# Optimization experiments

Measured on AMD Instinct MI355X. Metric: run time of the kernel, lower is better.

## Reference

```python
import jax, jax.numpy as jnp
import numpy as np

N = 50000      # nodes
E = 800000     # edges
IN = 128       # in_channels
H = 128        # hidden_channels
OUT = 40       # out_channels (classes)
EPS = 1e-5     # LayerNorm eps


def _glorot(key, fan_in, fan_out):
    lim = np.sqrt(6.0 / (fan_in + fan_out)).astype(np.float32)
    return jax.random.uniform(key, (fan_in, fan_out), jnp.float32, -lim, lim)


def setup_inputs() -> dict:
    key = jax.random.key(0)
    ks = jax.random.split(key, 8)
    x = jax.random.normal(ks[0], (N, IN), jnp.float32)
    edge_index = jax.random.randint(ks[1], (2, E), 0, N, jnp.int32)
    return {
        "x": x,
        "W0": _glorot(ks[2], IN, H), "b0": jnp.zeros((H,), jnp.float32),
        "W1": _glorot(ks[3], H, H),  "b1": jnp.zeros((H,), jnp.float32),
        "W2": _glorot(ks[4], H, OUT), "b2": jnp.zeros((OUT,), jnp.float32),
        "ln1_g": jnp.ones((H,), jnp.float32), "ln1_b": jnp.zeros((H,), jnp.float32),
        "ln2_g": jnp.ones((H,), jnp.float32), "ln2_b": jnp.zeros((H,), jnp.float32),
        "edge_index": edge_index,
    }


def reference(x, W0, b0, W1, b1, W2, b2, ln1_g, ln1_b, ln2_g, ln2_b, edge_index):
    # GCN normalization with self-loops: A_hat = D^-1/2 (A + I) D^-1/2
    self_idx = jnp.arange(N, dtype=edge_index.dtype)
    src = jnp.concatenate([edge_index[0], self_idx])  # [E+N]
    dst = jnp.concatenate([edge_index[1], self_idx])
    deg = jax.ops.segment_sum(jnp.ones_like(src, jnp.float32), dst, num_segments=N)
    dinv = jax.lax.rsqrt(deg)  # deg >= 1 thanks to self-loops
    norm = dinv[src] * dinv[dst]  # [E+N]

    def conv(h, W, b):
        h = h @ W                                  # [N, F] dense GEMM
        msg = h[src] * norm[:, None]               # gather + scale [E+N, F]
        return jax.ops.segment_sum(msg, dst, num_segments=N) + b

    def layernorm(h, g, b):
        mu = jnp.mean(h, axis=-1, keepdims=True)
        var = jnp.mean(jnp.square(h - mu), axis=-1, keepdims=True)
        return (h - mu) * jax.lax.rsqrt(var + EPS) * g + b

    # layer 0 (note: original uses lns[i+1], so lns[0] is never applied)
    h = jax.nn.relu(layernorm(conv(x, W0, b0), ln1_g, ln1_b))
    # dropout is identity in eval mode
    h = jax.nn.relu(layernorm(conv(h, W1, b1), ln2_g, ln2_b))
    h = conv(h, W2, b2)
    return jax.nn.log_softmax(h, axis=-1)
```

## Files before the change

### kernel.cpp

```cpp
#include <hip/hip_runtime.h>
#include <math.h>

typedef __attribute__((ext_vector_type(8))) short bf16x8;
typedef __attribute__((ext_vector_type(4))) float f32x4;
typedef unsigned short u16;
typedef unsigned int u32;

static __device__ __forceinline__ u16 f2bf(float f) {
    unsigned u = __float_as_uint(f);
    unsigned r = (u + 0x7fff + ((u >> 16) & 1)) >> 16;
    return (u16)r;
}
static __device__ __forceinline__ float bf2f(u16 h) {
    return __uint_as_float(((unsigned)h) << 16);
}
static __device__ __forceinline__ float pk_lo(u32 u) { return __uint_as_float(u << 16); }
static __device__ __forceinline__ float pk_hi(u32 u) { return __uint_as_float(u & 0xffff0000u); }

__global__ void init_k(int* __restrict__ counts, int n, int gN,
                       const float* __restrict__ W0, const float* __restrict__ W1,
                       const float* __restrict__ W2,
                       u16* __restrict__ w0hi, u16* __restrict__ w0lo,
                       u16* __restrict__ w1hi, u16* __restrict__ w1lo,
                       u16* __restrict__ w2hi, u16* __restrict__ w2lo) {
    int b = blockIdx.x;
    if (b < gN) {
        int i = b * 256 + threadIdx.x;
        if (i < n) counts[i] = 0;
        return;
    }
    int i = (b - gN) * 256 + threadIdx.x;
    const float* W; u16 *hi, *lo; int COLS, cin, idx;
    if (i < 16384)      { W = W0; hi = w0hi; lo = w0lo; COLS = 128; cin = 128; idx = i; }
    else if (i < 32768) { W = W1; hi = w1hi; lo = w1lo; COLS = 128; cin = 128; idx = i - 16384; }
    else if (i < 40960) { W = W2; hi = w2hi; lo = w2lo; COLS = 64;  cin = 40;  idx = i - 32768; }
    else return;
    int k = idx / COLS, col = idx % COLS;
    float v = (col < cin) ? W[k * cin + col] : 0.f;
    u16 h = f2bf(v);
    u16 l = f2bf(v - bf2f(h));
    int ct = col >> 4, ks = k >> 5, ln = (col & 15) + (((k >> 3) & 3) << 4), j = k & 7;
    int pos = (((ct * 4 + ks) * 64 + ln) << 3) + j;
    hi[pos] = h; lo[pos] = l;
}

__global__ void count_rank_k(const int* __restrict__ dst, int* __restrict__ counts,
                             u16* __restrict__ rank, int e) {
    int i = blockIdx.x * 256 + threadIdx.x;
    if (i < e) rank[i] = (u16)atomicAdd(&counts[dst[i]], 1);
}
__global__ __launch_bounds__(1024) void scan1_k(const int* __restrict__ counts,
                                                int* __restrict__ offs,
                                                int* __restrict__ bsum,
                                                float* __restrict__ dinv, int n) {
    __shared__ int ws[16];
    int tid = threadIdx.x;
    int i = blockIdx.x * 1024 + tid;
    int lane = tid & 63, w = tid >> 6;
    int c = (i < n) ? counts[i] : 0;
    if (i < n) dinv[i] = rsqrtf((float)c + 1.0f);
    int s = c;
#pragma unroll
    for (int o = 1; o < 64; o <<= 1) { int t = __shfl_up(s, o); if (lane >= o) s += t; }
    if (lane == 63) ws[w] = s;
    __syncthreads();
    if (w == 0) {
        int x = (lane < 16) ? ws[lane] : 0;
#pragma unroll
        for (int o = 1; o < 16; o <<= 1) { int t = __shfl_up(x, o); if (lane >= o) x += t; }
        if (lane < 16) ws[lane] = x;
    }
    __syncthreads();
    int base = (w > 0) ? ws[w - 1] : 0;
    int incl = base + s;
    if (i < n) offs[i + 1] = incl;
    if (tid == 1023) bsum[blockIdx.x] = incl;
}
__global__ void scan23_k(int* __restrict__ offs, const int* __restrict__ bsum,
                         int nb, int n) {
    __shared__ int pre[64];
    int tid = threadIdx.x;
    if (tid < 64) {
        int v = (tid < nb) ? bsum[tid] : 0;
#pragma unroll
        for (int o = 1; o < 64; o <<= 1) { int t = __shfl_up(v, o); if (tid >= o) v += t; }
        pre[tid] = v;
    }
    __syncthreads();
    int i = blockIdx.x * 256 + tid;
    if (i == 0) offs[0] = 0;
    if (i < n) {
        int b = i >> 10;
        offs[i + 1] += (b > 0) ? pre[b - 1] : 0;
    }
}

__global__ __launch_bounds__(256) void fill_gemm1_k(const int* __restrict__ src,
                                                    const int* __restrict__ dst,
                                                    const u16* __restrict__ rank,
                                                    const int* __restrict__ offs,
                                                    u16* __restrict__ csr, int e, int fillBlocks,
                                                    const float* __restrict__ A,
                                                    const u16* __restrict__ Whi,
                                                    const u16* __restrict__ Wlo,
                                                    const float* __restrict__ dinv,
                                                    u16* __restrict__ C, int nrows) {
    if ((int)blockIdx.x < fillBlocks) {
        int i = blockIdx.x * 256 + threadIdx.x;
        if (i < e) csr[offs[dst[i]] + (int)rank[i]] = (u16)src[i];
        return;
    }
    constexpr int COLS = 128;
    int bid = blockIdx.x - fillBlocks;
    int wave = threadIdx.x >> 6, lane = threadIdx.x & 63;
    int r0 = bid * 64 + wave * 16;
    int arow = min(r0 + (lane & 15), nrows - 1);
    int kbase = (lane >> 4) * 8;

    bf16x8 ahi[4], alo[4];
#pragma unroll
    for (int ks = 0; ks < 4; ++ks) {
        const float* ap = &A[(long)arow * 128 + ks * 32 + kbase];
        float4 f0 = *(const float4*)ap;
        float4 f1 = *(const float4*)(ap + 4);
        float fv[8] = {f0.x, f0.y, f0.z, f0.w, f1.x, f1.y, f1.z, f1.w};
#pragma unroll
        for (int j = 0; j < 8; ++j) {
            u16 h = f2bf(fv[j]);
            ahi[ks][j] = (short)h;
            alo[ks][j] = (short)f2bf(fv[j] - bf2f(h));
        }
    }
    float dscale[4];
#pragma unroll
    for (int r = 0; r < 4; ++r) {
        int orow = r0 + (lane >> 4) * 4 + r;
        dscale[r] = (orow < nrows) ? dinv[orow] : 0.f;
    }
#pragma unroll
    for (int ct = 0; ct < COLS / 16; ct += 2) {
        f32x4 acc0 = {0.f, 0.f, 0.f, 0.f}, acc1 = {0.f, 0.f, 0.f, 0.f};
#pragma unroll
        for (int ks = 0; ks < 4; ++ks) {
            int fo0 = ((ct * 4 + ks) * 64 + lane) * 8;
            int fo1 = (((ct + 1) * 4 + ks) * 64 + lane) * 8;
            bf16x8 bhi0 = *(const bf16x8*)&Whi[fo0];
            bf16x8 blo0 = *(const bf16x8*)&Wlo[fo0];
            bf16x8 bhi1 = *(const bf16x8*)&Whi[fo1];
            bf16x8 blo1 = *(const bf16x8*)&Wlo[fo1];
            acc0 = __builtin_amdgcn_mfma_f32_16x16x32_bf16(ahi[ks], bhi0, acc0, 0, 0, 0);
            acc1 = __builtin_amdgcn_mfma_f32_16x16x32_bf16(ahi[ks], bhi1, acc1, 0, 0, 0);
            acc0 = __builtin_amdgcn_mfma_f32_16x16x32_bf16(alo[ks], bhi0, acc0, 0, 0, 0);
            acc1 = __builtin_amdgcn_mfma_f32_16x16x32_bf16(alo[ks], bhi1, acc1, 0, 0, 0);
            acc0 = __builtin_amdgcn_mfma_f32_16x16x32_bf16(ahi[ks], blo0, acc0, 0, 0, 0);
            acc1 = __builtin_amdgcn_mfma_f32_16x16x32_bf16(ahi[ks], blo1, acc1, 0, 0, 0);
        }
#pragma unroll
        for (int r = 0; r < 4; ++r) {
            int orow = r0 + (lane >> 4) * 4 + r;
            if (orow < nrows) {
                C[(long)orow * COLS + ct * 16 + (lane & 15)] = f2bf(acc0[r] * dscale[r]);
                C[(long)orow * COLS + (ct + 1) * 16 + (lane & 15)] = f2bf(acc1[r] * dscale[r]);
            }
        }
    }
}

template<int COLS>
__global__ __launch_bounds__(256) void mfma_gemm_bf16a_k(const u16* __restrict__ A,
                                                         const u16* __restrict__ Whi,
                                                         const u16* __restrict__ Wlo,
                                                         const float* __restrict__ dinv,
                                                         u16* __restrict__ C, int nrows) {
    int wave = threadIdx.x >> 6, lane = threadIdx.x & 63;
    int r0 = blockIdx.x * 64 + wave * 16;
    int arow = min(r0 + (lane & 15), nrows - 1);
    int kbase = (lane >> 4) * 8;

    bf16x8 a[4];
#pragma unroll
    for (int ks = 0; ks < 4; ++ks)
        a[ks] = *(const bf16x8*)&A[(long)arow * 128 + ks * 32 + kbase];

    float dscale[4];
#pragma unroll
    for (int r = 0; r < 4; ++r) {
        int orow = r0 + (lane >> 4) * 4 + r;
        dscale[r] = (orow < nrows) ? dinv[orow] : 0.f;
    }
#pragma unroll
    for (int ct = 0; ct < COLS / 16; ct += 2) {
        f32x4 acc0 = {0.f, 0.f, 0.f, 0.f}, acc1 = {0.f, 0.f, 0.f, 0.f};
#pragma unroll
        for (int ks = 0; ks < 4; ++ks) {
            int fo0 = ((ct * 4 + ks) * 64 + lane) * 8;
            int fo1 = (((ct + 1) * 4 + ks) * 64 + lane) * 8;
            bf16x8 bhi0 = *(const bf16x8*)&Whi[fo0];
            bf16x8 blo0 = *(const bf16x8*)&Wlo[fo0];
            bf16x8 bhi1 = *(const bf16x8*)&Whi[fo1];
            bf16x8 blo1 = *(const bf16x8*)&Wlo[fo1];
            acc0 = __builtin_amdgcn_mfma_f32_16x16x32_bf16(a[ks], bhi0, acc0, 0, 0, 0);
            acc1 = __builtin_amdgcn_mfma_f32_16x16x32_bf16(a[ks], bhi1, acc1, 0, 0, 0);
            acc0 = __builtin_amdgcn_mfma_f32_16x16x32_bf16(a[ks], blo0, acc0, 0, 0, 0);
            acc1 = __builtin_amdgcn_mfma_f32_16x16x32_bf16(a[ks], blo1, acc1, 0, 0, 0);
        }
#pragma unroll
        for (int r = 0; r < 4; ++r) {
            int orow = r0 + (lane >> 4) * 4 + r;
            if (orow < nrows) {
                C[(long)orow * COLS + ct * 16 + (lane & 15)] = f2bf(acc0[r] * dscale[r]);
                C[(long)orow * COLS + (ct + 1) * 16 + (lane & 15)] = f2bf(acc1[r] * dscale[r]);
            }
        }
    }
}

__global__ __launch_bounds__(256) void agg_ln_relu_k(const u16* __restrict__ Cs,
                                                     const int* __restrict__ offs,
                                                     const u16* __restrict__ csr,
                                                     const float* __restrict__ dinv,
                                                     const float* __restrict__ bias,
                                                     const float* __restrict__ g,
                                                     const float* __restrict__ b,
                                                     u16* __restrict__ out, int n) {
    int wid = (blockIdx.x * 256 + threadIdx.x) >> 6;
    int lane = threadIdx.x & 63;
    if (wid >= n) return;
    const u32* C2 = (const u32*)Cs;
    u32 su = C2[(long)wid * 64 + lane];
    float axq[4], ayq[4];
    axq[0] = pk_lo(su); ayq[0] = pk_hi(su);
    axq[1] = axq[2] = axq[3] = 0.f;
    ayq[1] = ayq[2] = ayq[3] = 0.f;
    int beg = offs[wid], end = offs[wid + 1];
    int j = beg;
    while (j < end) {
        int take = min(64, end - j);
        int myidx = (lane < take) ? (int)csr[j + lane] : 0;
        int k = 0;
        for (; k + 16 <= take; k += 16) {
            int is[16];
#pragma unroll
            for (int q = 0; q < 16; ++q) is[q] = __shfl(myidx, k + q);
            u32 us[16];
#pragma unroll
            for (int q = 0; q < 16; ++q) us[q] = C2[(long)is[q] * 64 + lane];
#pragma unroll
            for (int q = 0; q < 16; ++q) {
                axq[q & 3] += pk_lo(us[q]);
                ayq[q & 3] += pk_hi(us[q]);
            }
        }
        for (; k + 8 <= take; k += 8) {
            int is[8];
#pragma unroll
            for (int q = 0; q < 8; ++q) is[q] = __shfl(myidx, k + q);
            u32 us[8];
#pragma unroll
            for (int q = 0; q < 8; ++q) us[q] = C2[(long)is[q] * 64 + lane];
#pragma unroll
            for (int q = 0; q < 8; ++q) {
                axq[q & 3] += pk_lo(us[q]);
                ayq[q & 3] += pk_hi(us[q]);
            }
        }
        for (; k < take; ++k) {
            int i0 = __shfl(myidx, k);
            u32 u0 = C2[(long)i0 * 64 + lane];
            axq[0] += pk_lo(u0); ayq[0] += pk_hi(u0);
        }
        j += take;
    }
    float ax = (axq[0] + axq[1]) + (axq[2] + axq[3]);
    float ay = (ayq[0] + ayq[1]) + (ayq[2] + ayq[3]);
    float w = dinv[wid];
    float2 bia = ((const float2*)bias)[lane];
    float t0 = ax * w + bia.x;
    float t1 = ay * w + bia.y;
    float s = t0 + t1;
#pragma unroll
    for (int off = 32; off; off >>= 1) s += __shfl_xor(s, off);
    float mu = s * (1.f / 128.f);
    float d0 = t0 - mu, d1 = t1 - mu;
    float v = d0 * d0 + d1 * d1;
#pragma unroll
    for (int off = 32; off; off >>= 1) v += __shfl_xor(v, off);
    float rstd = rsqrtf(v * (1.f / 128.f) + 1e-5f);
    float2 gv = ((const float2*)g)[lane];
    float2 bv = ((const float2*)b)[lane];
    float y0 = fmaxf(0.f, d0 * rstd * gv.x + bv.x);
    float y1 = fmaxf(0.f, d1 * rstd * gv.y + bv.y);
    ((u32*)out)[(long)wid * 64 + lane] = ((u32)f2bf(y1) << 16) | f2bf(y0);
}

__global__ __launch_bounds__(256) void agg_lsm_k(const u16* __restrict__ Cs,
                                                 const int* __restrict__ offs,
                                                 const u16* __restrict__ csr,
                                                 const float* __restrict__ dinv,
                                                 const float* __restrict__ b2,
                                                 float* __restrict__ out, int n) {
    int wid = (blockIdx.x * 256 + threadIdx.x) >> 6;
    int lane = threadIdx.x & 63;
    if (wid >= n) return;
    float aq[4];
    aq[0] = bf2f(Cs[(long)wid * 64 + lane]);
    aq[1] = aq[2] = aq[3] = 0.f;
    int beg = offs[wid], end = offs[wid + 1];
    int j = beg;
    while (j < end) {
        int take = min(64, end - j);
        int myidx = (lane < take) ? (int)csr[j + lane] : 0;
        int k = 0;
        for (; k + 16 <= take; k += 16) {
            int is[16];
#pragma unroll
            for (int q = 0; q < 16; ++q) is[q] = __shfl(myidx, k + q);
            u16 us[16];
#pragma unroll
            for (int q = 0; q < 16; ++q) us[q] = Cs[(long)is[q] * 64 + lane];
#pragma unroll
            for (int q = 0; q < 16; ++q) aq[q & 3] += bf2f(us[q]);
        }
        for (; k + 8 <= take; k += 8) {
            int is[8];
#pragma unroll
            for (int q = 0; q < 8; ++q) is[q] = __shfl(myidx, k + q);
            u16 us[8];
#pragma unroll
            for (int q = 0; q < 8; ++q) us[q] = Cs[(long)is[q] * 64 + lane];
#pragma unroll
            for (int q = 0; q < 8; ++q) aq[q & 3] += bf2f(us[q]);
        }
        for (; k < take; ++k) {
            int i0 = __shfl(myidx, k);
            aq[0] += bf2f(Cs[(long)i0 * 64 + lane]);
        }
        j += take;
    }
    float aa = (aq[0] + aq[1]) + (aq[2] + aq[3]);
    float v = (lane < 40) ? aa * dinv[wid] + b2[lane] : -INFINITY;
    float m = v;
#pragma unroll
    for (int off = 32; off; off >>= 1) m = fmaxf(m, __shfl_xor(m, off));
    float e = (lane < 40) ? expf(v - m) : 0.f;
    float s = e;
#pragma unroll
    for (int off = 32; off; off >>= 1) s += __shfl_xor(s, off);
    float r = v - m - logf(s);
    if (lane < 40) out[(long)wid * 40 + lane] = r;
}

extern "C" void kernel_launch(void* const* d_in, const int* in_sizes, int n_in,
                              void* d_out, int out_size, void* d_ws, size_t ws_size,
                              hipStream_t stream) {
    const float* x    = (const float*)d_in[0];
    const float* W0   = (const float*)d_in[1];
    const float* b0   = (const float*)d_in[2];
    const float* W1   = (const float*)d_in[3];
    const float* b1   = (const float*)d_in[4];
    const float* W2   = (const float*)d_in[5];
    const float* b2   = (const float*)d_in[6];
    const float* ln1g = (const float*)d_in[7];
    const float* ln1b = (const float*)d_in[8];
    const float* ln2g = (const float*)d_in[9];
    const float* ln2b = (const float*)d_in[10];
    const int*   ei   = (const int*)d_in[11];

    const int N = in_sizes[0] / 128;
    const int E = in_sizes[11] / 2;
    const int* esrc = ei;
    const int* edst = ei + E;
    float* out = (float*)d_out;

    const int Npad = ((N + 255) / 256) * 256;

    int* counts  = (int*)d_ws;
    int* offs    = counts + Npad;
    int* bsum    = offs + Npad;
    u16* rank16  = (u16*)(bsum + 64);
    u16* csr16   = rank16 + E;
    float* dinv  = (float*)(csr16 + E);
    u16* bufA    = (u16*)(dinv + Npad);
    u16* bufB    = bufA + (size_t)N * 128;
    u16* w0hi    = bufB + (size_t)N * 128;
    u16* w0lo    = w0hi + 16384;
    u16* w1hi    = w0lo + 16384;
    u16* w1lo    = w1hi + 16384;
    u16* w2hi    = w1lo + 16384;
    u16* w2lo    = w2hi + 8192;

    dim3 blk(256);
    int gN = (N + 255) / 256, gE = (E + 255) / 256;
    int nb1024 = (N + 1023) / 1024;
    int gG = (N + 63) / 64;
    int gW = (N + 3) / 4;

    init_k<<<gN + 160, blk, 0, stream>>>(counts, N, gN, W0, W1, W2,
                                         w0hi, w0lo, w1hi, w1lo, w2hi, w2lo);
    count_rank_k<<<gE, blk, 0, stream>>>(edst, counts, rank16, E);
    scan1_k<<<nb1024, 1024, 0, stream>>>(counts, offs, bsum, dinv, N);
    scan23_k<<<gN, blk, 0, stream>>>(offs, bsum, nb1024, N);
    fill_gemm1_k<<<gE + gG, blk, 0, stream>>>(esrc, edst, rank16, offs, csr16, E, gE,
                                              x, w0hi, w0lo, dinv, bufA, N);
    agg_ln_relu_k<<<gW, blk, 0, stream>>>(bufA, offs, csr16, dinv, b0, ln1g, ln1b, bufB, N);
    mfma_gemm_bf16a_k<128><<<gG, blk, 0, stream>>>(bufB, w1hi, w1lo, dinv, bufA, N);
    agg_ln_relu_k<<<gW, blk, 0, stream>>>(bufA, offs, csr16, dinv, b1, ln2g, ln2b, bufB, N);
    mfma_gemm_bf16a_k<64><<<gG, blk, 0, stream>>>(bufB, w2hi, w2lo, dinv, bufA, N);
    agg_lsm_k<<<gW, blk, 0, stream>>>(bufA, offs, csr16, dinv, b2, out, N);
}
```

Baseline: 211.4 us.

## Move first GEMM into count kernel and rescale with dinv in fill pass

The first-layer GEMM (x @ W0) now runs in the same launch as the edge-counting atomics, because it no longer needs dinv. It writes raw fp32 results to a scratch buffer. The CSR fill kernel then also applies the dinv row scaling and converts to bf16. This hides the GEMM behind the atomic-heavy counting pass, at the cost of an extra fp32 write and read of an N×128 intermediate (about 25 MB each way).

```diff
diff --git a/kernel.cpp b/kernel.cpp
--- a/kernel.cpp
+++ b/kernel.cpp
@@ -44,74 +44,20 @@
     hi[pos] = h; lo[pos] = l;
 }
 
-__global__ void count_rank_k(const int* __restrict__ dst, int* __restrict__ counts,
-                             u16* __restrict__ rank, int e) {
-    int i = blockIdx.x * 256 + threadIdx.x;
-    if (i < e) rank[i] = (u16)atomicAdd(&counts[dst[i]], 1);
-}
-__global__ __launch_bounds__(1024) void scan1_k(const int* __restrict__ counts,
-                                                int* __restrict__ offs,
-                                                int* __restrict__ bsum,
-                                                float* __restrict__ dinv, int n) {
-    __shared__ int ws[16];
-    int tid = threadIdx.x;
-    int i = blockIdx.x * 1024 + tid;
-    int lane = tid & 63, w = tid >> 6;
-    int c = (i < n) ? counts[i] : 0;
-    if (i < n) dinv[i] = rsqrtf((float)c + 1.0f);
-    int s = c;
-#pragma unroll
-    for (int o = 1; o < 64; o <<= 1) { int t = __shfl_up(s, o); if (lane >= o) s += t; }
-    if (lane == 63) ws[w] = s;
-    __syncthreads();
-    if (w == 0) {
-        int x = (lane < 16) ? ws[lane] : 0;
-#pragma unroll
-        for (int o = 1; o < 16; o <<= 1) { int t = __shfl_up(x, o); if (lane >= o) x += t; }
-        if (lane < 16) ws[lane] = x;
-    }
-    __syncthreads();
-    int base = (w > 0) ? ws[w - 1] : 0;
-    int incl = base + s;
-    if (i < n) offs[i + 1] = incl;
-    if (tid == 1023) bsum[blockIdx.x] = incl;
-}
-__global__ void scan23_k(int* __restrict__ offs, const int* __restrict__ bsum,
-                         int nb, int n) {
-    __shared__ int pre[64];
-    int tid = threadIdx.x;
-    if (tid < 64) {
-        int v = (tid < nb) ? bsum[tid] : 0;
-#pragma unroll
-        for (int o = 1; o < 64; o <<= 1) { int t = __shfl_up(v, o); if (tid >= o) v += t; }
-        pre[tid] = v;
-    }
-    __syncthreads();
-    int i = blockIdx.x * 256 + tid;
-    if (i == 0) offs[0] = 0;
-    if (i < n) {
-        int b = i >> 10;
-        offs[i + 1] += (b > 0) ? pre[b - 1] : 0;
-    }
-}
-
-__global__ __launch_bounds__(256) void fill_gemm1_k(const int* __restrict__ src,
-                                                    const int* __restrict__ dst,
-                                                    const u16* __restrict__ rank,
-                                                    const int* __restrict__ offs,
-                                                    u16* __restrict__ csr, int e, int fillBlocks,
-                                                    const float* __restrict__ A,
-                                                    const u16* __restrict__ Whi,
-                                                    const u16* __restrict__ Wlo,
-                                                    const float* __restrict__ dinv,
-                                                    u16* __restrict__ C, int nrows) {
-    if ((int)blockIdx.x < fillBlocks) {
+__global__ __launch_bounds__(256) void crg1_k(const int* __restrict__ dst,
+                                              int* __restrict__ counts,
+                                              u16* __restrict__ rank, int e, int cntBlocks,
+                                              const float* __restrict__ A,
+                                              const u16* __restrict__ Whi,
+                                              const u16* __restrict__ Wlo,
+                                              float* __restrict__ C, int nrows) {
+    if ((int)blockIdx.x < cntBlocks) {
         int i = blockIdx.x * 256 + threadIdx.x;
-        if (i < e) csr[offs[dst[i]] + (int)rank[i]] = (u16)src[i];
+        if (i < e) rank[i] = (u16)atomicAdd(&counts[dst[i]], 1);
         return;
     }
     constexpr int COLS = 128;
-    int bid = blockIdx.x - fillBlocks;
+    int bid = blockIdx.x - cntBlocks;
     int wave = threadIdx.x >> 6, lane = threadIdx.x & 63;
     int r0 = bid * 64 + wave * 16;
     int arow = min(r0 + (lane & 15), nrows - 1);
@@ -130,12 +76,6 @@
             ahi[ks][j] = (short)h;
             alo[ks][j] = (short)f2bf(fv[j] - bf2f(h));
         }
-    }
-    float dscale[4];
-#pragma unroll
-    for (int r = 0; r < 4; ++r) {
-        int orow = r0 + (lane >> 4) * 4 + r;
-        dscale[r] = (orow < nrows) ? dinv[orow] : 0.f;
     }
 #pragma unroll
     for (int ct = 0; ct < COLS / 16; ct += 2) {
@@ -159,11 +99,81 @@
         for (int r = 0; r < 4; ++r) {
             int orow = r0 + (lane >> 4) * 4 + r;
             if (orow < nrows) {
-                C[(long)orow * COLS + ct * 16 + (lane & 15)] = f2bf(acc0[r] * dscale[r]);
-                C[(long)orow * COLS + (ct + 1) * 16 + (lane & 15)] = f2bf(acc1[r] * dscale[r]);
+                C[(long)orow * COLS + ct * 16 + (lane & 15)] = acc0[r];
+                C[(long)orow * COLS + (ct + 1) * 16 + (lane & 15)] = acc1[r];
             }
         }
     }
+}
+
+__global__ __launch_bounds__(1024) void scan1_k(const int* __restrict__ counts,
+                                                int* __restrict__ offs,
+                                                int* __restrict__ bsum,
+                                                float* __restrict__ dinv, int n) {
+    __shared__ int ws[16];
+    int tid = threadIdx.x;
+    int i = blockIdx.x * 1024 + tid;
+    int lane = tid & 63, w = tid >> 6;
+    int c = (i < n) ? counts[i] : 0;
+    if (i < n) dinv[i] = rsqrtf((float)c + 1.0f);
+    int s = c;
+#pragma unroll
+    for (int o = 1; o < 64; o <<= 1) { int t = __shfl_up(s, o); if (lane >= o) s += t; }
+    if (lane == 63) ws[w] = s;
+    __syncthreads();
+    if (w == 0) {
+        int x = (lane < 16) ? ws[lane] : 0;
+#pragma unroll
+        for (int o = 1; o < 16; o <<= 1) { int t = __shfl_up(x, o); if (lane >= o) x += t; }
+        if (lane < 16) ws[lane] = x;
+    }
+    __syncthreads();
+    int base = (w > 0) ? ws[w - 1] : 0;
+    int incl = base + s;
+    if (i < n) offs[i + 1] = incl;
+    if (tid == 1023) bsum[blockIdx.x] = incl;
+}
+__global__ void scan23_k(int* __restrict__ offs, const int* __restrict__ bsum,
+                         int nb, int n) {
+    __shared__ int pre[64];
+    int tid = threadIdx.x;
+    if (tid < 64) {
+        int v = (tid < nb) ? bsum[tid] : 0;
+#pragma unroll
+        for (int o = 1; o < 64; o <<= 1) { int t = __shfl_up(v, o); if (tid >= o) v += t; }
+        pre[tid] = v;
+    }
+    __syncthreads();
+    int i = blockIdx.x * 256 + tid;
+    if (i == 0) offs[0] = 0;
+    if (i < n) {
+        int b = i >> 10;
+        offs[i + 1] += (b > 0) ? pre[b - 1] : 0;
+    }
+}
+
+__global__ __launch_bounds__(256) void fill_rescale_k(const int* __restrict__ src,
+                                                      const int* __restrict__ dst,
+                                                      const u16* __restrict__ rank,
+                                                      const int* __restrict__ offs,
+                                                      u16* __restrict__ csr, int e, int fillBlocks,
+                                                      const float* __restrict__ Craw,
+                                                      const float* __restrict__ dinv,
+                                                      u16* __restrict__ Cs, int n) {
+    if ((int)blockIdx.x < fillBlocks) {
+        int i = blockIdx.x * 256 + threadIdx.x;
+        if (i < e) csr[offs[dst[i]] + (int)rank[i]] = (u16)src[i];
+        return;
+    }
+    int t = (blockIdx.x - fillBlocks) * 256 + threadIdx.x;
+    if (t >= n * 32) return;
+    int row = t >> 5;
+    float w = dinv[row];
+    float4 v = ((const float4*)Craw)[t];
+    uint2 o2;
+    o2.x = ((u32)f2bf(v.y * w) << 16) | f2bf(v.x * w);
+    o2.y = ((u32)f2bf(v.w * w) << 16) | f2bf(v.z * w);
+    ((uint2*)Cs)[t] = o2;
 }
 
 template<int COLS>
@@ -381,8 +391,9 @@
     u16* csr16   = rank16 + E;
     float* dinv  = (float*)(csr16 + E);
     u16* bufA    = (u16*)(dinv + Npad);
-    u16* bufB    = bufA + (size_t)N * 128;
-    u16* w0hi    = bufB + (size_t)N * 128;
+    float* bufRaw = (float*)(bufA + (size_t)N * 128);
+    u16* bufB    = (u16*)bufRaw;
+    u16* w0hi    = (u16*)(bufRaw + (size_t)N * 128);
     u16* w0lo    = w0hi + 16384;
     u16* w1hi    = w0lo + 16384;
     u16* w1lo    = w1hi + 16384;
@@ -394,14 +405,16 @@
     int nb1024 = (N + 1023) / 1024;
     int gG = (N + 63) / 64;
     int gW = (N + 3) / 4;
+    int gR = (N * 32 + 255) / 256;
 
     init_k<<<gN + 160, blk, 0, stream>>>(counts, N, gN, W0, W1, W2,
                                          w0hi, w0lo, w1hi, w1lo, w2hi, w2lo);
-    count_rank_k<<<gE, blk, 0, stream>>>(edst, counts, rank16, E);
+    crg1_k<<<gE + gG, blk, 0, stream>>>(edst, counts, rank16, E, gE,
+                                        x, w0hi, w0lo, bufRaw, N);
     scan1_k<<<nb1024, 1024, 0, stream>>>(counts, offs, bsum, dinv, N);
     scan23_k<<<gN, blk, 0, stream>>>(offs, bsum, nb1024, N);
-    fill_gemm1_k<<<gE + gG, blk, 0, stream>>>(esrc, edst, rank16, offs, csr16, E, gE,
-                                              x, w0hi, w0lo, dinv, bufA, N);
+    fill_rescale_k<<<gE + gR, blk, 0, stream>>>(esrc, edst, rank16, offs, csr16, E, gE,
+                                                bufRaw, dinv, bufA, N);
     agg_ln_relu_k<<<gW, blk, 0, stream>>>(bufA, offs, csr16, dinv, b0, ln1g, ln1b, bufB, N);
     mfma_gemm_bf16a_k<128><<<gG, blk, 0, stream>>>(bufB, w1hi, w1lo, dinv, bufA, N);
     agg_ln_relu_k<<<gW, blk, 0, stream>>>(bufA, offs, csr16, dinv, b1, ln2g, ln2b, bufB, N);
```

After: 216.6 us. 2.4% more time.
